# Kernel tuning notes

Hardware: AMD Instinct MI355X
Metric: run time of the kernel (lower is better)

The kernel has to match this reference:

```python
import jax, jax.numpy as jnp
import numpy as np

LN_EPS = 1e-5


def setup_inputs() -> dict:
    key = jax.random.key(0)
    ks = jax.random.split(key, 6)
    B, L, H, N = 4, 4096, 1024, 64
    x = jax.random.normal(ks[0], (B, L, H), dtype=jnp.float32)
    gamma = jnp.ones((H,), dtype=jnp.float32)
    beta = jnp.zeros((H,), dtype=jnp.float32)
    LR = jax.random.normal(ks[1], (N,), dtype=jnp.float32)
    LI = jax.random.normal(ks[2], (N,), dtype=jnp.float32)
    CR = jax.random.normal(ks[3], (H, N), dtype=jnp.float32)
    CI = jax.random.normal(ks[4], (H, N), dtype=jnp.float32)
    D = jax.random.normal(ks[5], (H,), dtype=jnp.float32)
    return {"x": x, "gamma": gamma, "beta": beta, "LR": LR, "LI": LI,
            "CR": CR, "CI": CI, "D": D}


def reference(x, gamma, beta, LR, LI, CR, CI, D):
    # x: [B, L, H]
    L = x.shape[1]
    # LayerNorm over last dim
    mu = jnp.mean(x, axis=-1, keepdims=True)
    var = jnp.mean(jnp.square(x - mu), axis=-1, keepdims=True)
    xn = (x - mu) * jax.lax.rsqrt(var + LN_EPS) * gamma + beta
    # Diagonal state-space kernel (DSS)
    Lambda = -jnp.exp(LR) + 1j * jnp.exp(LI)            # [N] complex
    C = (CR + 1j * CI) * (jnp.exp(Lambda) - 1.0) / Lambda  # [H, N]
    # Vandermonde: S[n, l] = exp(Lambda[n] * l)
    pos = jnp.arange(L, dtype=jnp.float32)
    S = jnp.exp(Lambda[:, None] * pos[None, :])          # [N, L]
    K = jnp.einsum('hn,nl->lh', C, S).real               # [L, H]
    # Causal convolution via zero-padded FFT of length 2L
    n_fft = 2 * L
    K_f = jnp.fft.rfft(K, n=n_fft, axis=0)               # [L+1, H]
    u_f = jnp.fft.rfft(xn, n=n_fft, axis=1)              # [B, L+1, H]
    y = jnp.fft.irfft(u_f * K_f, n=n_fft, axis=1)[:, :L, :]
    return y + D * xn
```

## Files before the change

kernel.cpp:

```cpp
#include <hip/hip_runtime.h>
#include <hip/hip_bf16.h>

#define B_  4
#define L_  4096
#define H_  1024
#define N_  64
#define LN_EPS 1e-5f
#define SLOT 16384
#define KLEN 320
#define KROW 400
#define SN_L 32
#define TSTR 1034

typedef __bf16 bf16x8 __attribute__((ext_vector_type(8)));
typedef __bf16 bf16x4 __attribute__((ext_vector_type(4)));
typedef __bf16 bf16x2 __attribute__((ext_vector_type(2)));
typedef float  f32x4  __attribute__((ext_vector_type(4)));

#define MFMA(a, b, c) __builtin_amdgcn_mfma_f32_16x16x32_bf16((a), (b), (c), 0, 0, 0)

__global__ __launch_bounds__(512, 4) void k_A(
    const float* __restrict__ x,
    const float* __restrict__ gamma, const float* __restrict__ beta,
    const float* __restrict__ LR, const float* __restrict__ LI,
    const float* __restrict__ CR, const float* __restrict__ CI,
    const float* __restrict__ Dv,
    char* __restrict__ slab, __bf16* __restrict__ Krev8)
{
    __shared__ __attribute__((aligned(16))) char smem[66448];
    const int bid = blockIdx.x, t = threadIdx.x;
    const int m3 = bid % 3, q3 = bid / 3;

    if (m3 == 0) {
        __bf16 (*tile)[TSTR] = (__bf16(*)[TSTR])smem;
        float2* rstats = (float2*)(smem + SN_L * TSTR * 2);
        const int l0 = (q3 & 127) * SN_L, b = q3 >> 7;

        {
            int r = t >> 4, c16 = t & 15;
            const float* xrow = x + ((size_t)b * L_ + (l0 + r)) * H_;
            float s1 = 0.f, s2 = 0.f;
            #pragma unroll
            for (int k = 0; k < 16; ++k) {
                int h4 = c16 * 4 + 64 * k;
                float4 v = *(const float4*)&xrow[h4];
                s1 += v.x + v.y + v.z + v.w;
                s2 += v.x * v.x + v.y * v.y + v.z * v.z + v.w * v.w;
                bf16x2 lo = {(__bf16)v.x, (__bf16)v.y};
                bf16x2 hi = {(__bf16)v.z, (__bf16)v.w};
                *(bf16x2*)&tile[r][h4]     = lo;
                *(bf16x2*)&tile[r][h4 + 2] = hi;
            }
            #pragma unroll
            for (int off = 1; off < 16; off <<= 1) {
                s1 += __shfl_xor(s1, off, 64);
                s2 += __shfl_xor(s2, off, 64);
            }
            if ((t & 15) == 0) {
                float mu  = s1 * (1.0f / H_);
                float var = s2 * (1.0f / H_) - mu * mu;
                rstats[r] = make_float2(mu, rsqrtf(var + LN_EPS));
            }
        }
        __syncthreads();
        {
            int g = t & 3;
            float2 st[8];
            #pragma unroll
            for (int i = 0; i < 8; ++i) st[i] = rstats[8 * g + i];
            #pragma unroll
            for (int k = 0; k < 8; ++k) {
                int h = (t >> 2) + 128 * k;
                float gm = gamma[h], bt = beta[h];
                bf16x8 o;
                #pragma unroll
                for (int i = 0; i < 8; ++i) {
                    float xv = (float)tile[8 * g + i][h];
                    o[i] = (__bf16)((xv - st[i].x) * st[i].y * gm + bt);
                }
                __bf16* ub = (__bf16*)(slab + ((size_t)(b * H_ + h)) * SLOT + SLOT / 2);
                *(bf16x8*)&ub[l0 + 8 * g] = o;
            }
        }
    } else {
        float* lr_l  = (float*)smem;
        float* li_l  = lr_l + 64;
        float* crr_l = li_l + 64;
        float* cii_l = crr_l + 64;
        const int h = q3 * 2 + (m3 - 1);
        __bf16* row = Krev8 + (size_t)h * 8 * KROW;

        if (t < 64) {
            int n = t;
            float lr = -expf(LR[n]);
            float li =  expf(LI[n]);
            float er = expf(lr);
            float Er = er * cosf(li);
            float Ei = er * sinf(li);
            float nr = Er - 1.0f, ni = Ei;
            float inv = 1.0f / (lr * lr + li * li);
            float wr = (nr * lr + ni * li) * inv;
            float wi = (ni * lr - nr * li) * inv;
            float cr = CR[h * N_ + n], ci = CI[h * N_ + n];
            lr_l[n]  = lr;  li_l[n] = li;
            crr_l[n] = cr * wr - ci * wi;
            cii_l[n] = cr * wi + ci * wr;
        } else if (t >= 320) {
            for (int idx = t - 320; idx < 640; idx += 192) {
                int s = idx / 80, qq = idx - s * 80;
                int pos = (qq < s) ? qq : 320 + qq;
                row[s * KROW + pos] = (__bf16)0.0f;
            }
        }
        __syncthreads();
        if (t < KLEN) {
            float fd = (float)t;
            float k = 0.0f;
            #pragma unroll 8
            for (int n = 0; n < N_; ++n) {
                float e = __expf(fd * lr_l[n]);
                float c = __cosf(fd * li_l[n]);
                float s = __sinf(fd * li_l[n]);
                k = fmaf(crr_l[n], e * c, fmaf(-cii_l[n], e * s, k));
            }
            if (t == 0) k += Dv[h];
            __bf16 kb = (__bf16)k;
            #pragma unroll
            for (int s = 0; s < 8; ++s)
                row[s * KROW + s + (KLEN - 1 - t)] = kb;
        }
    }
}

__global__ __launch_bounds__(256, 8) void k_main(
    char* __restrict__ slab, const __bf16* __restrict__ Krev8)
{
    __shared__ __attribute__((aligned(16))) char smem[9792];
    __bf16 (*Upad)[72] = (__bf16(*)[72])smem;
    __bf16 (*Ylb)[72]  = (__bf16(*)[72])smem;

    const int bid = blockIdx.x;
    const int h = bid >> 2, b = bid & 3;
    const int R = b * H_ + h;
    const int tid = threadIdx.x;
    const int wv  = tid >> 6, ln = tid & 63;
    const int lrn = ln & 15, kg = ln >> 4;
    const int trow = wv * 16 + lrn;

    const __bf16* urow = (const __bf16*)(slab + (size_t)R * SLOT + SLOT / 2);
    __bf16* yrow = (__bf16*)(slab + (size_t)R * SLOT);

    uint4 u0 = *(const uint4*)(urow + tid * 16);
    uint4 u1 = *(const uint4*)(urow + tid * 16 + 8);

    const __bf16* krow = Krev8 + (size_t)h * 8 * KROW;
    bf16x8 af[5][2];
    #pragma unroll
    for (int d = 0; d < 5; ++d) {
        #pragma unroll
        for (int kap = 0; kap < 2; ++kap) {
            int base = (KLEN - 1) - 64 * d - trow + kap * 32 + kg * 8;
            int s = (-base) & 7;
            af[d][kap] = *(const bf16x8*)&krow[s * KROW + base + s];
        }
    }

    {
        int c = tid >> 2, j0 = (tid & 3) * 16;
        *(uint4*)&Upad[4 + c][j0]     = u0;
        *(uint4*)&Upad[4 + c][j0 + 8] = u1;
    }
    if (tid < 36) {
        uint4 z = {0u, 0u, 0u, 0u};
        *(uint4*)(smem + tid * 16) = z;
    }
    __syncthreads();

    f32x4 res[4];
    #pragma unroll
    for (int ct = 0; ct < 4; ++ct) {
        f32x4 acc = {0.f, 0.f, 0.f, 0.f};
        #pragma unroll
        for (int d = 0; d < 5; ++d) {
            int ur = ct * 16 + lrn + 4 - d;
            acc = MFMA(af[d][0], *(const bf16x8*)&Upad[ur][kg * 8],      acc);
            acc = MFMA(af[d][1], *(const bf16x8*)&Upad[ur][32 + kg * 8], acc);
        }
        res[ct] = acc;
    }
    __syncthreads();

    {
        int t0 = wv * 16 + kg * 4;
        #pragma unroll
        for (int ct = 0; ct < 4; ++ct) {
            bf16x4 rb = {(__bf16)res[ct][0], (__bf16)res[ct][1],
                         (__bf16)res[ct][2], (__bf16)res[ct][3]};
            *(bf16x4*)&Ylb[ct * 16 + lrn][t0] = rb;
        }
    }
    __syncthreads();
    {
        int c = tid >> 2, j0 = (tid & 3) * 16;
        bf16x8 o0 = *(const bf16x8*)&Ylb[c][j0];
        bf16x8 o1 = *(const bf16x8*)&Ylb[c][j0 + 8];
        *(bf16x8*)&yrow[c * 64 + j0]     = o0;
        *(bf16x8*)&yrow[c * 64 + j0 + 8] = o1;
    }
}

__global__ __launch_bounds__(256) void k_out(
    const char* __restrict__ slab, float* __restrict__ out)
{
    __shared__ float tile[64][68];
    int h0 = blockIdx.x * 64, l0 = blockIdx.y * 64, b = blockIdx.z;
    int t = threadIdx.x;

    int hyb = t >> 3;
    int l8  = (t & 7) * 8;
    #pragma unroll
    for (int p = 0; p < 2; ++p) {
        int hy = hyb + 32 * p;
        const __bf16* yb = (const __bf16*)(slab + ((size_t)(b * H_ + h0 + hy)) * SLOT);
        bf16x8 v = *(const bf16x8*)&yb[l0 + l8];
        #pragma unroll
        for (int i = 0; i < 8; ++i) {
            int l = l8 + i;
            tile[l][hy ^ ((l >> 3) << 2)] = (float)v[i];
        }
    }
    __syncthreads();

    int hq  = (t & 15) * 4;
    int lyb = t >> 4;
    #pragma unroll
    for (int p = 0; p < 4; ++p) {
        int ly = lyb + p * 16;
        f32x4 v = *(const f32x4*)&tile[ly][hq ^ ((ly >> 3) << 2)];
        *(f32x4*)&out[((size_t)b * L_ + (l0 + ly)) * H_ + h0 + hq] = v;
    }
}

extern "C" void kernel_launch(void* const* d_in, const int* in_sizes, int n_in,
                              void* d_out, int out_size, void* d_ws, size_t ws_size,
                              hipStream_t stream)
{
    const float* x     = (const float*)d_in[0];
    const float* gamma = (const float*)d_in[1];
    const float* beta  = (const float*)d_in[2];
    const float* LR    = (const float*)d_in[3];
    const float* LI    = (const float*)d_in[4];
    const float* CR    = (const float*)d_in[5];
    const float* CI    = (const float*)d_in[6];
    const float* D     = (const float*)d_in[7];
    float* out = (float*)d_out;

    const size_t BHL = (size_t)B_ * H_ * L_;

    char*   slab  = (char*)d_ws;
    __bf16* Krev8 = (__bf16*)(slab + BHL * 4);

    k_A   <<<dim3(1536),            dim3(512), 0, stream>>>(
        x, gamma, beta, LR, LI, CR, CI, D, slab, Krev8);
    k_main<<<dim3(B_ * H_),         dim3(256), 0, stream>>>(slab, Krev8);
    k_out <<<dim3(H_/64, L_/64, B_), dim3(256), 0, stream>>>(slab, out);
}
```

Measured before the change: 64.48 us.

## Fuse Toeplitz MFMA convolution with output transpose into one kernel

Merges the per-row MFMA convolution kernel and the bf16-to-fp32 transpose kernel into a single kernel. Each block handles 16 channels by 1024 positions, loads the shifted input chunks into shared memory, runs the Toeplitz MFMA with the kernel taps as the A operand streamed from global, and writes fp32 output directly. This removes the bf16 y round-trip through the workspace and one launch. In exchange, kernel fragments are reloaded per output tile and the output stores are only 16-byte segments per row across channels.

Measured after the change: 81.28 us. +26.0%, slower.

```diff
diff --git a/kernel.cpp b/kernel.cpp
--- a/kernel.cpp
+++ b/kernel.cpp
@@ -11,6 +11,10 @@
 #define KROW 400
 #define SN_L 32
 #define TSTR 1034
+#define HG   16
+#define UCH  20
+#define USTR 72
+#define YSTR 68
 
 typedef __bf16 bf16x8 __attribute__((ext_vector_type(8)));
 typedef __bf16 bf16x4 __attribute__((ext_vector_type(4)));
@@ -132,112 +136,81 @@
     }
 }
 
-__global__ __launch_bounds__(256, 8) void k_main(
-    char* __restrict__ slab, const __bf16* __restrict__ Krev8)
+__global__ __launch_bounds__(512, 4) void k_fused(
+    const char* __restrict__ slab, const __bf16* __restrict__ Krev8,
+    float* __restrict__ out)
 {
-    __shared__ __attribute__((aligned(16))) char smem[9792];
-    __bf16 (*Upad)[72] = (__bf16(*)[72])smem;
-    __bf16 (*Ylb)[72]  = (__bf16(*)[72])smem;
-
-    const int bid = blockIdx.x;
-    const int h = bid >> 2, b = bid & 3;
-    const int R = b * H_ + h;
-    const int tid = threadIdx.x;
-    const int wv  = tid >> 6, ln = tid & 63;
+    __shared__ __attribute__((aligned(16))) char smem[HG*UCH*USTR*2 + HG*16*YSTR*2];
+    __bf16 (*U)[UCH][USTR] = (__bf16(*)[UCH][USTR])smem;
+    __bf16 (*Y)[16][YSTR]  = (__bf16(*)[16][YSTR])(smem + HG*UCH*USTR*2);
+
+    const int h0 = blockIdx.x * HG;
+    const int cg = blockIdx.y;
+    const int b  = blockIdx.z;
+    const int t  = threadIdx.x;
+    const int w  = t >> 6, ln = t & 63;
     const int lrn = ln & 15, kg = ln >> 4;
-    const int trow = wv * 16 + lrn;
-
-    const __bf16* urow = (const __bf16*)(slab + (size_t)R * SLOT + SLOT / 2);
-    __bf16* yrow = (__bf16*)(slab + (size_t)R * SLOT);
-
-    uint4 u0 = *(const uint4*)(urow + tid * 16);
-    uint4 u1 = *(const uint4*)(urow + tid * 16 + 8);
-
-    const __bf16* krow = Krev8 + (size_t)h * 8 * KROW;
-    bf16x8 af[5][2];
+
+    {
+        const char* ubase = slab + ((size_t)(b * H_ + h0)) * SLOT + SLOT / 2;
+        const long src_off = (long)cg * 2048 - 512;
+        #pragma unroll
+        for (int i = 0; i < 5; ++i) {
+            int f = t + i * 512;
+            int hl = f / 160, q = f - hl * 160;
+            uint4 v;
+            if (cg == 0 && q < 32) v = make_uint4(0u, 0u, 0u, 0u);
+            else v = *(const uint4*)(ubase + (size_t)hl * SLOT + src_off + q * 16);
+            *(uint4*)((char*)&U[hl][0][0] + (q >> 3) * (USTR * 2) + (q & 7) * 16) = v;
+        }
+    }
+    __syncthreads();
+
     #pragma unroll
-    for (int d = 0; d < 5; ++d) {
-        #pragma unroll
-        for (int kap = 0; kap < 2; ++kap) {
-            int base = (KLEN - 1) - 64 * d - trow + kap * 32 + kg * 8;
-            int s = (-base) & 7;
-            af[d][kap] = *(const bf16x8*)&krow[s * KROW + base + s];
-        }
-    }
+    for (int hh = 0; hh < 2; ++hh) {
+        const int hl = w * 2 + hh;
+        const __bf16* krow = Krev8 + (size_t)(h0 + hl) * 8 * KROW;
+        bf16x8 bfr[5][2];
+        #pragma unroll
+        for (int d = 0; d < 5; ++d) {
+            int ur = lrn + 4 - d;
+            bfr[d][0] = *(const bf16x8*)&U[hl][ur][kg * 8];
+            bfr[d][1] = *(const bf16x8*)&U[hl][ur][32 + kg * 8];
+        }
+        #pragma unroll
+        for (int mt = 0; mt < 4; ++mt) {
+            const int trow = mt * 16 + lrn;
+            f32x4 acc = {0.f, 0.f, 0.f, 0.f};
+            #pragma unroll
+            for (int d = 0; d < 5; ++d) {
+                #pragma unroll
+                for (int kap = 0; kap < 2; ++kap) {
+                    int bas = (KLEN - 1) - 64 * d - trow + kap * 32 + kg * 8;
+                    int s = (-bas) & 7;
+                    bf16x8 af = *(const bf16x8*)&krow[s * KROW + bas + s];
+                    acc = MFMA(af, bfr[d][kap], acc);
+                }
+            }
+            bf16x4 rb = {(__bf16)acc[0], (__bf16)acc[1],
+                         (__bf16)acc[2], (__bf16)acc[3]};
+            *(bf16x4*)&Y[hl][lrn][mt * 16 + kg * 4] = rb;
+        }
+    }
+    __syncthreads();
 
     {
-        int c = tid >> 2, j0 = (tid & 3) * 16;
-        *(uint4*)&Upad[4 + c][j0]     = u0;
-        *(uint4*)&Upad[4 + c][j0 + 8] = u1;
-    }
-    if (tid < 36) {
-        uint4 z = {0u, 0u, 0u, 0u};
-        *(uint4*)(smem + tid * 16) = z;
-    }
-    __syncthreads();
-
-    f32x4 res[4];
-    #pragma unroll
-    for (int ct = 0; ct < 4; ++ct) {
-        f32x4 acc = {0.f, 0.f, 0.f, 0.f};
-        #pragma unroll
-        for (int d = 0; d < 5; ++d) {
-            int ur = ct * 16 + lrn + 4 - d;
-            acc = MFMA(af[d][0], *(const bf16x8*)&Upad[ur][kg * 8],      acc);
-            acc = MFMA(af[d][1], *(const bf16x8*)&Upad[ur][32 + kg * 8], acc);
-        }
-        res[ct] = acc;
-    }
-    __syncthreads();
-
-    {
-        int t0 = wv * 16 + kg * 4;
-        #pragma unroll
-        for (int ct = 0; ct < 4; ++ct) {
-            bf16x4 rb = {(__bf16)res[ct][0], (__bf16)res[ct][1],
-                         (__bf16)res[ct][2], (__bf16)res[ct][3]};
-            *(bf16x4*)&Ylb[ct * 16 + lrn][t0] = rb;
-        }
-    }
-    __syncthreads();
-    {
-        int c = tid >> 2, j0 = (tid & 3) * 16;
-        bf16x8 o0 = *(const bf16x8*)&Ylb[c][j0];
-        bf16x8 o1 = *(const bf16x8*)&Ylb[c][j0 + 8];
-        *(bf16x8*)&yrow[c * 64 + j0]     = o0;
-        *(bf16x8*)&yrow[c * 64 + j0 + 8] = o1;
-    }
-}
-
-__global__ __launch_bounds__(256) void k_out(
-    const char* __restrict__ slab, float* __restrict__ out)
-{
-    __shared__ float tile[64][68];
-    int h0 = blockIdx.x * 64, l0 = blockIdx.y * 64, b = blockIdx.z;
-    int t = threadIdx.x;
-
-    int hyb = t >> 3;
-    int l8  = (t & 7) * 8;
-    #pragma unroll
-    for (int p = 0; p < 2; ++p) {
-        int hy = hyb + 32 * p;
-        const __bf16* yb = (const __bf16*)(slab + ((size_t)(b * H_ + h0 + hy)) * SLOT);
-        bf16x8 v = *(const bf16x8*)&yb[l0 + l8];
+        const int g = t & 3, lr0 = t >> 2;
         #pragma unroll
         for (int i = 0; i < 8; ++i) {
-            int l = l8 + i;
-            tile[l][hy ^ ((l >> 3) << 2)] = (float)v[i];
-        }
-    }
-    __syncthreads();
-
-    int hq  = (t & 15) * 4;
-    int lyb = t >> 4;
-    #pragma unroll
-    for (int p = 0; p < 4; ++p) {
-        int ly = lyb + p * 16;
-        f32x4 v = *(const f32x4*)&tile[ly][hq ^ ((ly >> 3) << 2)];
-        *(f32x4*)&out[((size_t)b * L_ + (l0 + ly)) * H_ + h0 + hq] = v;
+            int l = lr0 + i * 128;
+            int c = l >> 6, tp = l & 63;
+            f32x4 v;
+            v[0] = (float)Y[g * 4 + 0][c][tp];
+            v[1] = (float)Y[g * 4 + 1][c][tp];
+            v[2] = (float)Y[g * 4 + 2][c][tp];
+            v[3] = (float)Y[g * 4 + 3][c][tp];
+            *(f32x4*)&out[((size_t)b * L_ + cg * 1024 + l) * H_ + h0 + g * 4] = v;
+        }
     }
 }
 
@@ -260,8 +233,7 @@
     char*   slab  = (char*)d_ws;
     __bf16* Krev8 = (__bf16*)(slab + BHL * 4);
 
-    k_A   <<<dim3(1536),            dim3(512), 0, stream>>>(
+    k_A    <<<dim3(1536),               dim3(512), 0, stream>>>(
         x, gamma, beta, LR, LI, CR, CI, D, slab, Krev8);
-    k_main<<<dim3(B_ * H_),         dim3(256), 0, stream>>>(slab, Krev8);
-    k_out <<<dim3(H_/64, L_/64, B_), dim3(256), 0, stream>>>(slab, out);
+    k_fused<<<dim3(H_/HG, L_/1024, B_), dim3(512), 0, stream>>>(slab, Krev8, out);
 }
```
